# Kernel optimization log

Measured on AMD Instinct MI355X. Metric: run time of the kernel, lower is better.

Reference implementation:

```python
import jax, jax.numpy as jnp
import numpy as np

N_NODES = 50000
N_EDGES = 300000
DIM = 256
ALPHA = 0.1  # residual mixing with initial features, as passed in forward


def gcn_layer(x0, x, edge_idx, W):
    """One GraphConvolution call: mean neighbor aggregation over the edge
    list, GCNII-style residual mix with initial features x0, then linear."""
    src, dst = edge_idx[0], edge_idx[1]
    msgs = x[src]  # [E, D] gather
    agg = jax.ops.segment_sum(msgs, dst, num_segments=x.shape[0])
    deg = jax.ops.segment_sum(jnp.ones((src.shape[0],), x.dtype), dst,
                              num_segments=x.shape[0])
    agg = agg / jnp.maximum(deg, 1.0)[:, None]
    h = ALPHA * x0 + (1.0 - ALPHA) * agg
    return h @ W


def setup_inputs() -> dict:
    key = jax.random.key(0)
    k1, k2, k3 = jax.random.split(key, 3)
    x = jax.random.normal(k1, (N_NODES, DIM), dtype=jnp.float32)
    edge_idx = jax.random.randint(k2, (2, N_EDGES), 0, N_NODES, dtype=jnp.int64)
    W = jax.random.normal(k3, (DIM, DIM), dtype=jnp.float32) / np.sqrt(DIM)
    return {"drug_cell_pair_feature": x, "edge_idx": edge_idx, "W": W}


def reference(drug_cell_pair_feature, edge_idx, W):
    x0 = drug_cell_pair_feature
    out = jax.nn.relu(gcn_layer(x0, x0, edge_idx, W))
    for _ in range(4):  # 4 more identical calls, always mixing with x0
        out = jax.nn.relu(gcn_layer(x0, out, edge_idx, W))
    return out
```

## Files before the change

kernel.cpp:

```cpp
#include <hip/hip_runtime.h>

#define DIM 256
#define SCAN_B 256

typedef __attribute__((ext_vector_type(8))) short short8;
typedef __attribute__((ext_vector_type(4))) float f32x4;

__device__ __forceinline__ unsigned short f32_to_bf16(float x) {
    unsigned int u = __float_as_uint(x);
    unsigned int r = u + 0x7FFFu + ((u >> 16) & 1u);
    return (unsigned short)(r >> 16);
}
__device__ __forceinline__ float bf16_to_f32(unsigned short h) {
    return __uint_as_float(((unsigned int)h) << 16);
}

__device__ __forceinline__ void load_lds16(const void* g, void* l) {
    __builtin_amdgcn_global_load_lds(
        (const __attribute__((address_space(1))) unsigned int*)g,
        (__attribute__((address_space(3))) unsigned int*)l, 16, 0, 0);
}

__global__ void deg_kernel(const int* __restrict__ dst, int E, int* __restrict__ deg) {
    int e = blockIdx.x * blockDim.x + threadIdx.x;
    if (e < E) atomicAdd(&deg[dst[e]], 1);
}

__global__ void invdeg_kernel(const int* __restrict__ deg, int N, float* __restrict__ inv_deg) {
    int n = blockIdx.x * blockDim.x + threadIdx.x;
    if (n < N) inv_deg[n] = 1.0f / (float)max(deg[n], 1);
}

__global__ void scan1_kernel(const int* __restrict__ deg, int N,
                             int* __restrict__ excl, int* __restrict__ bsums) {
    __shared__ int s[SCAN_B];
    int tid = threadIdx.x;
    int i = blockIdx.x * SCAN_B + tid;
    int v = (i < N) ? deg[i] : 0;
    s[tid] = v;
    __syncthreads();
    #pragma unroll
    for (int off = 1; off < SCAN_B; off <<= 1) {
        int t = (tid >= off) ? s[tid - off] : 0;
        __syncthreads();
        s[tid] += t;
        __syncthreads();
    }
    if (i <= N) excl[i] = s[tid] - v;
    if (tid == SCAN_B - 1) bsums[blockIdx.x] = s[tid];
}

__global__ void scan2_kernel(int* __restrict__ bsums, int nb) {
    __shared__ int s[SCAN_B];
    int tid = threadIdx.x;
    int v = (tid < nb) ? bsums[tid] : 0;
    s[tid] = v;
    __syncthreads();
    #pragma unroll
    for (int off = 1; off < SCAN_B; off <<= 1) {
        int t = (tid >= off) ? s[tid - off] : 0;
        __syncthreads();
        s[tid] += t;
        __syncthreads();
    }
    if (tid < nb) bsums[tid] = s[tid] - v;
}

__global__ void scan3_kernel(const int* __restrict__ excl, const int* __restrict__ bsums,
                             int N, int* __restrict__ row_start) {
    int i = blockIdx.x * SCAN_B + threadIdx.x;
    if (i <= N) row_start[i] = excl[i] + bsums[blockIdx.x];
}

__global__ void fill_kernel(const int* __restrict__ src, const int* __restrict__ dst, int E,
                            const int* __restrict__ row_start, int* __restrict__ cursor,
                            int* __restrict__ csr_src) {
    int e = blockIdx.x * blockDim.x + threadIdx.x;
    if (e < E) {
        int d = dst[e];
        int pos = row_start[d] + atomicAdd(&cursor[d], 1);
        csr_src[pos] = src[e];
    }
}

__global__ void wprep_kernel(const float* __restrict__ W,
                             unsigned short* __restrict__ Wt_hi,
                             unsigned short* __restrict__ Wt_lo) {
    int k = blockIdx.x;
    int n = threadIdx.x;
    float w = W[k * DIM + n];
    unsigned short hi = f32_to_bf16(w);
    float rem = w - bf16_to_f32(hi);
    Wt_hi[n * DIM + k] = hi;
    Wt_lo[n * DIM + k] = f32_to_bf16(rem);
}

__global__ void xprep_kernel(const float* __restrict__ x, unsigned short* __restrict__ act,
                             unsigned short* __restrict__ x0b, int n4) {
    int i = blockIdx.x * blockDim.x + threadIdx.x;
    if (i < n4) {
        float4 v = ((const float4*)x)[i];
        ushort4 o;
        o.x = f32_to_bf16(v.x); o.y = f32_to_bf16(v.y);
        o.z = f32_to_bf16(v.z); o.w = f32_to_bf16(v.w);
        ((ushort4*)act)[i] = o;
        ((ushort4*)x0b)[i] = o;
    }
}

__global__ __launch_bounds__(256) void aggregate_kernel(
    const unsigned short* __restrict__ xh, const unsigned short* __restrict__ x0b,
    const int* __restrict__ row_start, const int* __restrict__ csr_src,
    const float* __restrict__ inv_deg,
    unsigned short* __restrict__ h, int N)
{
    int node = blockIdx.x * 4 + (threadIdx.x >> 6);
    if (node >= N) return;
    int c = (threadIdx.x & 63) * 4;

    int beg = row_start[node];
    int end = row_start[node + 1];

    float a0 = 0.f, a1 = 0.f, a2 = 0.f, a3 = 0.f;
    int e = beg;
    for (; e + 2 <= end; e += 2) {
        int s0 = csr_src[e];
        int s1 = csr_src[e + 1];
        ushort4 v0 = *(const ushort4*)(xh + (size_t)s0 * DIM + c);
        ushort4 v1 = *(const ushort4*)(xh + (size_t)s1 * DIM + c);
        a0 += bf16_to_f32(v0.x) + bf16_to_f32(v1.x);
        a1 += bf16_to_f32(v0.y) + bf16_to_f32(v1.y);
        a2 += bf16_to_f32(v0.z) + bf16_to_f32(v1.z);
        a3 += bf16_to_f32(v0.w) + bf16_to_f32(v1.w);
    }
    if (e < end) {
        int s0 = csr_src[e];
        ushort4 v0 = *(const ushort4*)(xh + (size_t)s0 * DIM + c);
        a0 += bf16_to_f32(v0.x);
        a1 += bf16_to_f32(v0.y);
        a2 += bf16_to_f32(v0.z);
        a3 += bf16_to_f32(v0.w);
    }

    float scale = 0.9f * inv_deg[node];
    ushort4 xv = *(const ushort4*)(x0b + (size_t)node * DIM + c);
    ushort4 o;
    o.x = f32_to_bf16(0.1f * bf16_to_f32(xv.x) + scale * a0);
    o.y = f32_to_bf16(0.1f * bf16_to_f32(xv.y) + scale * a1);
    o.z = f32_to_bf16(0.1f * bf16_to_f32(xv.z) + scale * a2);
    o.w = f32_to_bf16(0.1f * bf16_to_f32(xv.w) + scale * a3);
    *(ushort4*)(h + (size_t)node * DIM + c) = o;
}

template <bool LAST>
__global__ __launch_bounds__(256) void gemm_kernel(
    const unsigned short* __restrict__ h,
    const unsigned short* __restrict__ Wt_hi, const unsigned short* __restrict__ Wt_lo,
    float* __restrict__ out_f32, unsigned short* __restrict__ out_bf16, int N)
{
    __shared__ unsigned short As[128 * 32];
    __shared__ unsigned short Bs_hi[128 * 32];
    __shared__ unsigned short Bs_lo[128 * 32];

    const int t    = threadIdx.x;
    const int w    = t >> 6;
    const int lane = t & 63;
    const int lm   = lane & 15;
    const int q    = lane >> 4;
    const int wm   = w >> 1, wn = w & 1;
    const int m0   = blockIdx.x * 128;
    const int n0   = blockIdx.y * 128;

    const int sr = t >> 2;
    const int sg = (t & 3) * 8;

    f32x4 acc[4][4];
    #pragma unroll
    for (int mi = 0; mi < 4; mi++)
        #pragma unroll
        for (int ni = 0; ni < 4; ni++)
            acc[mi][ni] = (f32x4){0.f, 0.f, 0.f, 0.f};

    for (int kb = 0; kb < DIM; kb += 32) {
        __syncthreads();
        #pragma unroll
        for (int half = 0; half < 2; half++) {
            int r = half * 64 + sr;
            int ldso = (half * 256 + t) * 8;
            load_lds16(h     + (size_t)(m0 + r) * DIM + kb + sg, &As[ldso]);
            load_lds16(Wt_hi + (size_t)(n0 + r) * DIM + kb + sg, &Bs_hi[ldso]);
            load_lds16(Wt_lo + (size_t)(n0 + r) * DIM + kb + sg, &Bs_lo[ldso]);
        }
        __syncthreads();

        short8 a[4];
        #pragma unroll
        for (int mi = 0; mi < 4; mi++) {
            int row = wm * 64 + mi * 16 + lm;
            a[mi] = *(const short8*)&As[row * 32 + q * 8];
        }
        #pragma unroll
        for (int ni = 0; ni < 4; ni++) {
            int row = wn * 64 + ni * 16 + lm;
            short8 b_hi = *(const short8*)&Bs_hi[row * 32 + q * 8];
            short8 b_lo = *(const short8*)&Bs_lo[row * 32 + q * 8];
            #pragma unroll
            for (int mi = 0; mi < 4; mi++) {
                acc[mi][ni] = __builtin_amdgcn_mfma_f32_16x16x32_bf16(a[mi], b_hi, acc[mi][ni], 0, 0, 0);
                acc[mi][ni] = __builtin_amdgcn_mfma_f32_16x16x32_bf16(a[mi], b_lo, acc[mi][ni], 0, 0, 0);
            }
        }
    }

    #pragma unroll
    for (int mi = 0; mi < 4; mi++) {
        const int rowb = m0 + wm * 64 + mi * 16 + q * 4;
        #pragma unroll
        for (int ni = 0; ni < 4; ni++) {
            const int col = n0 + wn * 64 + ni * 16 + lm;
            #pragma unroll
            for (int r = 0; r < 4; r++) {
                int row = rowb + r;
                if (row < N) {
                    float v = fmaxf(acc[mi][ni][r], 0.0f);
                    if (LAST) out_f32[(size_t)row * DIM + col] = v;
                    else      out_bf16[(size_t)row * DIM + col] = f32_to_bf16(v);
                }
            }
        }
    }
}

extern "C" void kernel_launch(void* const* d_in, const int* in_sizes, int n_in,
                              void* d_out, int out_size, void* d_ws, size_t ws_size,
                              hipStream_t stream) {
    const float* x0  = (const float*)d_in[0];
    const int*   ei  = (const int*)d_in[1];
    const float* W   = (const float*)d_in[2];
    float*       out = (float*)d_out;

    const int N = in_sizes[0] / DIM;
    const int E = in_sizes[1] / 2;
    const int N_pad = (N + 127) & ~127;
    const int* src = ei;
    const int* dst = ei + E;

    const int nb = (N + 1 + SCAN_B - 1) / SCAN_B;

    char* ws = (char*)d_ws;
    size_t off = 0;
    auto alloc = [&](size_t bytes) { char* p = ws + off; off += (bytes + 15) & ~size_t(15); return p; };
    unsigned short* h       = (unsigned short*)alloc((size_t)N_pad * DIM * 2);
    unsigned short* act     = (unsigned short*)alloc((size_t)N_pad * DIM * 2);
    unsigned short* x0b     = (unsigned short*)alloc((size_t)N_pad * DIM * 2);
    unsigned short* Wt_hi   = (unsigned short*)alloc((size_t)DIM * DIM * 2);
    unsigned short* Wt_lo   = (unsigned short*)alloc((size_t)DIM * DIM * 2);
    float* inv_deg  = (float*)alloc((size_t)N * 4);
    int*   deg      = (int*)  alloc((size_t)N * 4);
    int*   row_start= (int*)  alloc((size_t)(N + 1) * 4);
    int*   excl     = (int*)  alloc((size_t)(N + 1) * 4);
    int*   cursor   = (int*)  alloc((size_t)N * 4);
    int*   bsums    = (int*)  alloc((size_t)nb * 4);
    int*   csr_src  = (int*)  alloc((size_t)E * 4);

    hipMemsetAsync(deg, 0, (size_t)N * 4, stream);
    hipMemsetAsync(cursor, 0, (size_t)N * 4, stream);
    deg_kernel<<<(E + 255) / 256, 256, 0, stream>>>(dst, E, deg);
    invdeg_kernel<<<(N + 255) / 256, 256, 0, stream>>>(deg, N, inv_deg);
    scan1_kernel<<<nb, SCAN_B, 0, stream>>>(deg, N, excl, bsums);
    scan2_kernel<<<1, SCAN_B, 0, stream>>>(bsums, nb);
    scan3_kernel<<<nb, SCAN_B, 0, stream>>>(excl, bsums, N, row_start);
    fill_kernel<<<(E + 255) / 256, 256, 0, stream>>>(src, dst, E, row_start, cursor, csr_src);
    wprep_kernel<<<DIM, DIM, 0, stream>>>(W, Wt_hi, Wt_lo);
    const int n4 = N * DIM / 4;
    xprep_kernel<<<(n4 + 255) / 256, 256, 0, stream>>>(x0, act, x0b, n4);

    dim3 ggrid(N_pad / 128, 2);
    for (int layer = 0; layer < 5; layer++) {
        aggregate_kernel<<<(N + 3) / 4, 256, 0, stream>>>(act, x0b, row_start, csr_src,
                                                          inv_deg, h, N);
        if (layer == 4)
            gemm_kernel<true><<<ggrid, 256, 0, stream>>>(h, Wt_hi, Wt_lo, out, nullptr, N);
        else
            gemm_kernel<false><<<ggrid, 256, 0, stream>>>(h, Wt_hi, Wt_lo, nullptr, act, N);
    }
}
```

Measured before the change: 442.9 us.

## Drop split-bf16 weight GEMM, unroll aggregation by four, fold invdeg into scan

Replaces the hi/lo split bf16 representation of W with a single bf16 weight, which halves the MFMA count and the B-tile LDS traffic in the GEMM. Unrolls the neighbor gather loop to four independent loads per iteration for more memory-level parallelism. Also merges the inverse-degree computation into scan3 to remove one kernel launch. The GEMM loses precision because W is rounded to bf16, which could hurt accuracy across the five layers.

```diff
diff --git a/kernel.cpp b/kernel.cpp
--- a/kernel.cpp
+++ b/kernel.cpp
@@ -24,11 +24,6 @@
 __global__ void deg_kernel(const int* __restrict__ dst, int E, int* __restrict__ deg) {
     int e = blockIdx.x * blockDim.x + threadIdx.x;
     if (e < E) atomicAdd(&deg[dst[e]], 1);
-}
-
-__global__ void invdeg_kernel(const int* __restrict__ deg, int N, float* __restrict__ inv_deg) {
-    int n = blockIdx.x * blockDim.x + threadIdx.x;
-    if (n < N) inv_deg[n] = 1.0f / (float)max(deg[n], 1);
 }
 
 __global__ void scan1_kernel(const int* __restrict__ deg, int N,
@@ -67,9 +62,11 @@
 }
 
 __global__ void scan3_kernel(const int* __restrict__ excl, const int* __restrict__ bsums,
-                             int N, int* __restrict__ row_start) {
+                             const int* __restrict__ deg, int N,
+                             int* __restrict__ row_start, float* __restrict__ inv_deg) {
     int i = blockIdx.x * SCAN_B + threadIdx.x;
     if (i <= N) row_start[i] = excl[i] + bsums[blockIdx.x];
+    if (i < N) inv_deg[i] = 1.0f / (float)max(deg[i], 1);
 }
 
 __global__ void fill_kernel(const int* __restrict__ src, const int* __restrict__ dst, int E,
@@ -83,16 +80,10 @@
     }
 }
 
-__global__ void wprep_kernel(const float* __restrict__ W,
-                             unsigned short* __restrict__ Wt_hi,
-                             unsigned short* __restrict__ Wt_lo) {
+__global__ void wprep_kernel(const float* __restrict__ W, unsigned short* __restrict__ Wt) {
     int k = blockIdx.x;
     int n = threadIdx.x;
-    float w = W[k * DIM + n];
-    unsigned short hi = f32_to_bf16(w);
-    float rem = w - bf16_to_f32(hi);
-    Wt_hi[n * DIM + k] = hi;
-    Wt_lo[n * DIM + k] = f32_to_bf16(rem);
+    Wt[n * DIM + k] = f32_to_bf16(W[k * DIM + n]);
 }
 
 __global__ void xprep_kernel(const float* __restrict__ x, unsigned short* __restrict__ act,
@@ -123,17 +114,21 @@
 
     float a0 = 0.f, a1 = 0.f, a2 = 0.f, a3 = 0.f;
     int e = beg;
-    for (; e + 2 <= end; e += 2) {
+    for (; e + 4 <= end; e += 4) {
         int s0 = csr_src[e];
         int s1 = csr_src[e + 1];
+        int s2 = csr_src[e + 2];
+        int s3 = csr_src[e + 3];
         ushort4 v0 = *(const ushort4*)(xh + (size_t)s0 * DIM + c);
         ushort4 v1 = *(const ushort4*)(xh + (size_t)s1 * DIM + c);
-        a0 += bf16_to_f32(v0.x) + bf16_to_f32(v1.x);
-        a1 += bf16_to_f32(v0.y) + bf16_to_f32(v1.y);
-        a2 += bf16_to_f32(v0.z) + bf16_to_f32(v1.z);
-        a3 += bf16_to_f32(v0.w) + bf16_to_f32(v1.w);
-    }
-    if (e < end) {
+        ushort4 v2 = *(const ushort4*)(xh + (size_t)s2 * DIM + c);
+        ushort4 v3 = *(const ushort4*)(xh + (size_t)s3 * DIM + c);
+        a0 += (bf16_to_f32(v0.x) + bf16_to_f32(v1.x)) + (bf16_to_f32(v2.x) + bf16_to_f32(v3.x));
+        a1 += (bf16_to_f32(v0.y) + bf16_to_f32(v1.y)) + (bf16_to_f32(v2.y) + bf16_to_f32(v3.y));
+        a2 += (bf16_to_f32(v0.z) + bf16_to_f32(v1.z)) + (bf16_to_f32(v2.z) + bf16_to_f32(v3.z));
+        a3 += (bf16_to_f32(v0.w) + bf16_to_f32(v1.w)) + (bf16_to_f32(v2.w) + bf16_to_f32(v3.w));
+    }
+    for (; e < end; e++) {
         int s0 = csr_src[e];
         ushort4 v0 = *(const ushort4*)(xh + (size_t)s0 * DIM + c);
         a0 += bf16_to_f32(v0.x);
@@ -154,13 +149,11 @@
 
 template <bool LAST>
 __global__ __launch_bounds__(256) void gemm_kernel(
-    const unsigned short* __restrict__ h,
-    const unsigned short* __restrict__ Wt_hi, const unsigned short* __restrict__ Wt_lo,
+    const unsigned short* __restrict__ h, const unsigned short* __restrict__ Wt,
     float* __restrict__ out_f32, unsigned short* __restrict__ out_bf16, int N)
 {
     __shared__ unsigned short As[128 * 32];
-    __shared__ unsigned short Bs_hi[128 * 32];
-    __shared__ unsigned short Bs_lo[128 * 32];
+    __shared__ unsigned short Bs[128 * 32];
 
     const int t    = threadIdx.x;
     const int w    = t >> 6;
@@ -187,9 +180,8 @@
         for (int half = 0; half < 2; half++) {
             int r = half * 64 + sr;
             int ldso = (half * 256 + t) * 8;
-            load_lds16(h     + (size_t)(m0 + r) * DIM + kb + sg, &As[ldso]);
-            load_lds16(Wt_hi + (size_t)(n0 + r) * DIM + kb + sg, &Bs_hi[ldso]);
-            load_lds16(Wt_lo + (size_t)(n0 + r) * DIM + kb + sg, &Bs_lo[ldso]);
+            load_lds16(h  + (size_t)(m0 + r) * DIM + kb + sg, &As[ldso]);
+            load_lds16(Wt + (size_t)(n0 + r) * DIM + kb + sg, &Bs[ldso]);
         }
         __syncthreads();
 
@@ -202,13 +194,10 @@
         #pragma unroll
         for (int ni = 0; ni < 4; ni++) {
             int row = wn * 64 + ni * 16 + lm;
-            short8 b_hi = *(const short8*)&Bs_hi[row * 32 + q * 8];
-            short8 b_lo = *(const short8*)&Bs_lo[row * 32 + q * 8];
+            short8 b = *(const short8*)&Bs[row * 32 + q * 8];
             #pragma unroll
-            for (int mi = 0; mi < 4; mi++) {
-                acc[mi][ni] = __builtin_amdgcn_mfma_f32_16x16x32_bf16(a[mi], b_hi, acc[mi][ni], 0, 0, 0);
-                acc[mi][ni] = __builtin_amdgcn_mfma_f32_16x16x32_bf16(a[mi], b_lo, acc[mi][ni], 0, 0, 0);
-            }
+            for (int mi = 0; mi < 4; mi++)
+                acc[mi][ni] = __builtin_amdgcn_mfma_f32_16x16x32_bf16(a[mi], b, acc[mi][ni], 0, 0, 0);
         }
     }
 
@@ -253,8 +242,7 @@
     unsigned short* h       = (unsigned short*)alloc((size_t)N_pad * DIM * 2);
     unsigned short* act     = (unsigned short*)alloc((size_t)N_pad * DIM * 2);
     unsigned short* x0b     = (unsigned short*)alloc((size_t)N_pad * DIM * 2);
-    unsigned short* Wt_hi   = (unsigned short*)alloc((size_t)DIM * DIM * 2);
-    unsigned short* Wt_lo   = (unsigned short*)alloc((size_t)DIM * DIM * 2);
+    unsigned short* Wt      = (unsigned short*)alloc((size_t)DIM * DIM * 2);
     float* inv_deg  = (float*)alloc((size_t)N * 4);
     int*   deg      = (int*)  alloc((size_t)N * 4);
     int*   row_start= (int*)  alloc((size_t)(N + 1) * 4);
@@ -266,12 +254,11 @@
     hipMemsetAsync(deg, 0, (size_t)N * 4, stream);
     hipMemsetAsync(cursor, 0, (size_t)N * 4, stream);
     deg_kernel<<<(E + 255) / 256, 256, 0, stream>>>(dst, E, deg);
-    invdeg_kernel<<<(N + 255) / 256, 256, 0, stream>>>(deg, N, inv_deg);
     scan1_kernel<<<nb, SCAN_B, 0, stream>>>(deg, N, excl, bsums);
     scan2_kernel<<<1, SCAN_B, 0, stream>>>(bsums, nb);
-    scan3_kernel<<<nb, SCAN_B, 0, stream>>>(excl, bsums, N, row_start);
+    scan3_kernel<<<nb, SCAN_B, 0, stream>>>(excl, bsums, deg, N, row_start, inv_deg);
     fill_kernel<<<(E + 255) / 256, 256, 0, stream>>>(src, dst, E, row_start, cursor, csr_src);
-    wprep_kernel<<<DIM, DIM, 0, stream>>>(W, Wt_hi, Wt_lo);
+    wprep_kernel<<<DIM, DIM, 0, stream>>>(W, Wt);
     const int n4 = N * DIM / 4;
     xprep_kernel<<<(n4 + 255) / 256, 256, 0, stream>>>(x0, act, x0b, n4);
 
@@ -280,8 +267,8 @@
         aggregate_kernel<<<(N + 3) / 4, 256, 0, stream>>>(act, x0b, row_start, csr_src,
                                                           inv_deg, h, N);
         if (layer == 4)
-            gemm_kernel<true><<<ggrid, 256, 0, stream>>>(h, Wt_hi, Wt_lo, out, nullptr, N);
+            gemm_kernel<true><<<ggrid, 256, 0, stream>>>(h, Wt, out, nullptr, N);
         else
-            gemm_kernel<false><<<ggrid, 256, 0, stream>>>(h, Wt_hi, Wt_lo, nullptr, act, N);
-    }
-}
+            gemm_kernel<false><<<ggrid, 256, 0, stream>>>(h, Wt, nullptr, act, N);
+    }
+}
```

New measurement: 396.0 us. 10.6% less time.
